# Kernel tuning notes

Measured on AMD Instinct MI355X. Metric: run time of the kernel, lower is better.

## Reference

```python
import jax, jax.numpy as jnp
import numpy as np
from jax import lax

D = 512        # datapathSize (= slow-net hidden size = embedding size)
H = 20         # nonlinearAfterSlowHiddenSize
V = 32000      # softmaxOutputHeadSize = xEmbeddingsNum
T = 1024       # sequence length (number of sequential fast-weight updates)


def setup_inputs() -> dict:
    key = jax.random.key(0)
    ks = jax.random.split(key, 12)
    inp = {}
    inp["tokens"] = jax.random.randint(ks[0], (T,), 0, V)
    inp["targets"] = jax.random.randint(ks[1], (T,), 0, V)
    # learned parameters
    inp["embed"] = jax.random.normal(ks[2], (V, D), dtype=jnp.float32)
    # fastWeightsInit = rand(D,D) * (1/D)
    inp["fw_init"] = jax.random.uniform(ks[3], (D, D), dtype=jnp.float32) * (1.0 / D)
    inp["eta"] = jnp.array(1.0, dtype=jnp.float32)
    inp["wa"] = jax.random.normal(ks[4], (D, D), dtype=jnp.float32) * 0.05
    inp["wb"] = jax.random.normal(ks[5], (D, D), dtype=jnp.float32) * 0.05
    # nonlinearAfterSlow: Linear(D,H) -> selu -> Linear(H,D); stored as (in,out)
    lim_a = 1.0 / np.sqrt(D)
    inp["mlp_aw"] = jax.random.uniform(ks[6], (D, H), dtype=jnp.float32, minval=-lim_a, maxval=lim_a)
    inp["mlp_ab"] = jax.random.uniform(ks[7], (H,), dtype=jnp.float32, minval=-lim_a, maxval=lim_a)
    lim_b = 1.0 / np.sqrt(H)
    inp["mlp_bw"] = jax.random.uniform(ks[8], (H, D), dtype=jnp.float32, minval=-lim_b, maxval=lim_b)
    inp["mlp_bb"] = jax.random.uniform(ks[9], (D,), dtype=jnp.float32, minval=-lim_b, maxval=lim_b)
    # logit head Linear(D, V)
    inp["head_w"] = jax.random.uniform(ks[10], (D, V), dtype=jnp.float32, minval=-lim_a, maxval=lim_a)
    inp["head_b"] = jax.random.uniform(ks[11], (V,), dtype=jnp.float32, minval=-lim_a, maxval=lim_a)
    return inp


def reference(tokens, targets, embed, fw_init, eta, wa, wb,
              mlp_aw, mlp_ab, mlp_bw, mlp_bb, head_w, head_b):
    xs = embed[tokens]  # [T, D]

    def step(fw, x):
        # SlowNetB.forwardAndUpdate for one token
        z0 = x @ wa                      # [D]
        z1 = x @ wb                      # [D]
        fw_new = jnp.tanh(fw + eta * jnp.outer(z0, z1))  # [D, D]
        y = x @ fw_new                   # [D]
        return fw_new, y

    _, ys = lax.scan(step, fw_init, xs)  # ys: [T, D]

    # NonlinearLayer (batched over T)
    h = jax.nn.selu(ys @ mlp_aw + mlp_ab) @ mlp_bw + mlp_bb  # [T, D]
    mixed = 0.5 * h + 0.5 * xs
    logits = mixed @ head_w + head_b     # [T, V]

    logp = jax.nn.log_softmax(logits, axis=-1)
    loss = -jnp.mean(jnp.take_along_axis(logp, targets[:, None], axis=1))
    return logits, loss
```

## Files before the change

kernel.cpp:

```cpp
#include <hip/hip_runtime.h>

#define D 512
#define H 20
#define V 32000
#define T 1024

typedef unsigned int uint;
typedef unsigned short ushort_t;
typedef __attribute__((ext_vector_type(8))) short short8;
typedef __attribute__((ext_vector_type(4))) float floatx4;

__device__ __forceinline__ unsigned short f2bf(float f) {
    unsigned u = __builtin_bit_cast(unsigned, f);
    u += 0x7fffu + ((u >> 16) & 1u);
    return (unsigned short)(u >> 16);
}

__device__ __forceinline__ float tanh_fast(float x) {
    float t = __builtin_amdgcn_exp2f(x * 2.8853900817779268f);
    float r = __builtin_amdgcn_rcpf(t + 1.0f);
    return __builtin_fmaf(-2.0f, r, 1.0f);
}

__global__ __launch_bounds__(256) void gather_kernel(const int* __restrict__ tokens,
                                                     const float* __restrict__ embed,
                                                     float* __restrict__ xs) {
    int idx = blockIdx.x * 256 + threadIdx.x;
    int row = idx >> 7;
    int c   = idx & 127;
    float4 v = ((const float4*)(embed + (long)tokens[row] * D))[c];
    ((float4*)xs)[idx] = v;
}

__global__ __launch_bounds__(256) void zgemm_kernel(const float* __restrict__ xs,
                                                    const float* __restrict__ wa,
                                                    const float* __restrict__ wb,
                                                    float* __restrict__ z0,
                                                    float* __restrict__ z1) {
    __shared__ float Xs[16 * 68];
    __shared__ float Ws[16 * 68];
    const int tid = threadIdx.x;
    const int n0 = blockIdx.x * 64, m0 = blockIdx.y * 64;
    const float* Wm = blockIdx.z ? wb : wa;
    float* Z = blockIdx.z ? z1 : z0;
    const int tx = tid & 15, ty = tid >> 4;
    const int xrow = tid >> 2, xkc = (tid & 3) * 4;
    const int wrow = tid >> 4, wc = (tid & 15) * 4;
    float acc[4][4] = {};
    for (int k0 = 0; k0 < D; k0 += 16) {
        float4 xv = *(const float4*)(xs + (long)(m0 + xrow) * D + k0 + xkc);
        float4 wv = *(const float4*)(Wm + (long)(k0 + wrow) * D + n0 + wc);
        Xs[(xkc + 0) * 68 + xrow] = xv.x;
        Xs[(xkc + 1) * 68 + xrow] = xv.y;
        Xs[(xkc + 2) * 68 + xrow] = xv.z;
        Xs[(xkc + 3) * 68 + xrow] = xv.w;
        *(float4*)(Ws + wrow * 68 + wc) = wv;
        __syncthreads();
#pragma unroll
        for (int k = 0; k < 16; k++) {
            float4 a = *(const float4*)(Xs + k * 68 + ty * 4);
            float4 b = *(const float4*)(Ws + k * 68 + tx * 4);
            float av[4] = {a.x, a.y, a.z, a.w};
            float bv[4] = {b.x, b.y, b.z, b.w};
#pragma unroll
            for (int r = 0; r < 4; r++)
#pragma unroll
                for (int c = 0; c < 4; c++)
                    acc[r][c] = __builtin_fmaf(av[r], bv[c], acc[r][c]);
        }
        __syncthreads();
    }
#pragma unroll
    for (int r = 0; r < 4; r++) {
        float4 v = {acc[r][0], acc[r][1], acc[r][2], acc[r][3]};
        *(float4*)(Z + (long)(m0 + ty * 4 + r) * D + n0 + tx * 4) = v;
    }
}

__global__ __launch_bounds__(512) void scan_kernel(const float* __restrict__ z0,
                                                   const float* __restrict__ z1,
                                                   const float* __restrict__ xs,
                                                   const float* __restrict__ fw_init,
                                                   const float* __restrict__ eta_p,
                                                   float* __restrict__ y) {
    const int tid = threadIdx.x;
    const int jj = tid & 1, ii = tid >> 1;
    const int j0 = blockIdx.x * 2;
    const int j = j0 + jj;
    const int wv = tid >> 6, lane = tid & 63;
    __shared__ float part[8 * 8 * 2];
    const float eta = *eta_p;
    float f0 = fw_init[(long)ii * D + j];
    float f1 = fw_init[(long)(ii + 256) * D + j];
    for (int t0 = 0; t0 < T; t0 += 8) {
        float za[8], zb[8], xa[8], xb[8], ez[8];
#pragma unroll
        for (int c = 0; c < 8; c++) {
            const long tr = (long)(t0 + c) * D;
            za[c] = z0[tr + ii];
            zb[c] = z0[tr + ii + 256];
            xa[c] = xs[tr + ii];
            xb[c] = xs[tr + ii + 256];
            ez[c] = z1[tr + j];
        }
        float p[8];
#pragma unroll
        for (int c = 0; c < 8; c++) {
            float e = eta * ez[c];
            f0 = tanh_fast(__builtin_fmaf(e, za[c], f0));
            f1 = tanh_fast(__builtin_fmaf(e, zb[c], f1));
            p[c] = xa[c] * f0 + xb[c] * f1;
        }
#pragma unroll
        for (int c = 0; c < 8; c++) {
            float v = p[c];
#pragma unroll
            for (int m = 2; m <= 32; m <<= 1) v += __shfl_xor(v, m, 64);
            p[c] = v;
        }
        if (lane < 2) {
#pragma unroll
            for (int c = 0; c < 8; c++) part[c * 16 + wv * 2 + lane] = p[c];
        }
        __syncthreads();
        if (tid < 16) {
            int c = tid >> 1, jx = tid & 1;
            float s = 0.f;
#pragma unroll
            for (int w = 0; w < 8; w++) s += part[c * 16 + w * 2 + jx];
            y[(long)(t0 + c) * D + j0 + jx] = s;
        }
        __syncthreads();
    }
}

__global__ __launch_bounds__(64) void mlp_mix_kernel(const float* __restrict__ y,
                                                     const float* __restrict__ xs,
                                                     const float* __restrict__ Aw,
                                                     const float* __restrict__ Ab,
                                                     const float* __restrict__ Bw,
                                                     const float* __restrict__ Bb,
                                                     unsigned short* __restrict__ mixed) {
    const int t = blockIdx.x, lane = threadIdx.x;
    __shared__ float Alds[H * D];
    __shared__ float h[H];
    for (int f = lane; f < H * D; f += 64) {
        float v = Aw[f];
        int d = f / H, j = f - d * H;
        Alds[j * D + d] = v;
    }
    float yr[8];
#pragma unroll
    for (int s = 0; s < 8; s++) yr[s] = y[(long)t * D + s * 64 + lane];
    __syncthreads();
    const float sc = 1.0507009873554805f, al = 1.6732632423543772f;
    for (int j = 0; j < H; j++) {
        float a = 0.f;
#pragma unroll
        for (int s = 0; s < 8; s++) a = __builtin_fmaf(yr[s], Alds[j * D + s * 64 + lane], a);
#pragma unroll
        for (int m = 1; m <= 32; m <<= 1) a += __shfl_xor(a, m, 64);
        if (lane == 0) {
            a += Ab[j];
            h[j] = a > 0.f ? sc * a : sc * al * (__expf(a) - 1.f);
        }
    }
    __syncthreads();
#pragma unroll
    for (int s = 0; s < 8; s++) {
        int d = s * 64 + lane;
        float o = Bb[d];
#pragma unroll
        for (int j = 0; j < H; j++) o = __builtin_fmaf(h[j], Bw[j * D + d], o);
        float mx = 0.5f * o + 0.5f * xs[(long)t * D + d];
        mixed[(long)t * D + d] = f2bf(mx);
    }
}

__global__ __launch_bounds__(256) void convert_wt_kernel(const float* __restrict__ head_w,
                                                         unsigned short* __restrict__ wt) {
    __shared__ float tile[64 * 68];
    const int n0 = blockIdx.x * 64, k0 = blockIdx.y * 64;
    const int tid = threadIdx.x;
#pragma unroll
    for (int s = 0; s < 4; s++) {
        int idx4 = s * 256 + tid;
        int r = idx4 >> 4, c4 = idx4 & 15;
        float4 v = *(const float4*)(head_w + (long)(k0 + r) * V + n0 + c4 * 4);
        *(float4*)(tile + r * 68 + c4 * 4) = v;
    }
    __syncthreads();
    const int rr = tid >> 2;
    const int cq = tid & 3;
    uint u[8];
#pragma unroll
    for (int p = 0; p < 8; p++) {
        float a = tile[(cq * 16 + p * 2 + 0) * 68 + rr];
        float b = tile[(cq * 16 + p * 2 + 1) * 68 + rr];
        u[p] = (uint)f2bf(a) | ((uint)f2bf(b) << 16);
    }
    unsigned short* ob = wt + (long)(n0 + rr) * D + k0 + cq * 16;
    uint4 v0 = {u[0], u[1], u[2], u[3]};
    uint4 v1 = {u[4], u[5], u[6], u[7]};
    *(uint4*)ob = v0;
    *((uint4*)ob + 1) = v1;
}

__global__ __launch_bounds__(256) void head_gemm_kernel(const unsigned short* __restrict__ A,
                                                        const unsigned short* __restrict__ Bt,
                                                        const float* __restrict__ bias,
                                                        float* __restrict__ C) {
    __shared__ unsigned short As[128 * 64];
    __shared__ unsigned short Bs[128 * 64];
    const int tid = threadIdx.x;
    const int mt = blockIdx.x & 7, nt = blockIdx.x >> 3;
    const int m0 = mt * 128, n0 = nt * 128;
    const int wave = tid >> 6, lane = tid & 63;
    const int wm = wave >> 1, wn = wave & 1;
    const int quad = lane >> 4, l15 = lane & 15;
    floatx4 acc[4][4] = {};
    for (int k0 = 0; k0 < D; k0 += 64) {
#pragma unroll
        for (int s = 0; s < 4; s++) {
            int idx = s * 256 + tid;
            int row = idx >> 3, slot = idx & 7;
            int gch = slot ^ (row & 7);
            const unsigned short* ga = A + (long)(m0 + row) * D + k0 + gch * 8;
            __builtin_amdgcn_global_load_lds(
                (const __attribute__((address_space(1))) unsigned int*)ga,
                (__attribute__((address_space(3))) unsigned int*)(As + idx * 8), 16, 0, 0);
            const unsigned short* gb = Bt + (long)(n0 + row) * D + k0 + gch * 8;
            __builtin_amdgcn_global_load_lds(
                (const __attribute__((address_space(1))) unsigned int*)gb,
                (__attribute__((address_space(3))) unsigned int*)(Bs + idx * 8), 16, 0, 0);
        }
        __syncthreads();
#pragma unroll
        for (int ks = 0; ks < 2; ks++) {
            short8 af[4], bfr[4];
            int q = ks * 4 + quad;
#pragma unroll
            for (int f = 0; f < 4; f++) {
                int ar = wm * 64 + f * 16 + l15;
                af[f] = *(const short8*)(As + ar * 64 + ((q ^ (ar & 7)) * 8));
                int br = wn * 64 + f * 16 + l15;
                bfr[f] = *(const short8*)(Bs + br * 64 + ((q ^ (br & 7)) * 8));
            }
#pragma unroll
            for (int fr = 0; fr < 4; fr++)
#pragma unroll
                for (int fc = 0; fc < 4; fc++)
                    acc[fr][fc] = __builtin_amdgcn_mfma_f32_16x16x32_bf16(af[fr], bfr[fc],
                                                                          acc[fr][fc], 0, 0, 0);
        }
        __syncthreads();
    }
#pragma unroll
    for (int fc = 0; fc < 4; fc++) {
        int n = n0 + wn * 64 + fc * 16 + l15;
        float b = bias[n];
#pragma unroll
        for (int fr = 0; fr < 4; fr++) {
            int mr = m0 + wm * 64 + fr * 16 + quad * 4;
#pragma unroll
            for (int r = 0; r < 4; r++)
                C[(long)(mr + r) * V + n] = acc[fr][fc][r] + b;
        }
    }
}

__device__ __forceinline__ void lse_upd(float& m, float& s, float v) {
    if (v > m) { s = s * __expf(m - v) + 1.f; m = v; }
    else       { s += __expf(v - m); }
}
__device__ __forceinline__ void lse_comb(float& m, float& s, float m2, float s2) {
    float M = fmaxf(m, m2);
    s = s * __expf(m - M) + s2 * __expf(m2 - M);
    m = M;
}

__global__ __launch_bounds__(256) void loss_rows_kernel(const float* __restrict__ logits,
                                                        const int* __restrict__ targets,
                                                        float* __restrict__ ws_loss) {
    const int t = blockIdx.x, tid = threadIdx.x;
    const float4* row = (const float4*)(logits + (long)t * V);
    float m = -INFINITY, s = 0.f;
    for (int i = tid; i < V / 4; i += 256) {
        float4 v = row[i];
        lse_upd(m, s, v.x); lse_upd(m, s, v.y); lse_upd(m, s, v.z); lse_upd(m, s, v.w);
    }
#pragma unroll
    for (int msk = 1; msk <= 32; msk <<= 1) {
        float m2 = __shfl_xor(m, msk, 64);
        float s2 = __shfl_xor(s, msk, 64);
        lse_comb(m, s, m2, s2);
    }
    __shared__ float sm[4], ss[4];
    if ((tid & 63) == 0) { sm[tid >> 6] = m; ss[tid >> 6] = s; }
    __syncthreads();
    if (tid == 0) {
        float M = sm[0], S = ss[0];
#pragma unroll
        for (int w = 1; w < 4; w++) lse_comb(M, S, sm[w], ss[w]);
        float lse = M + __logf(S);
        float lt = logits[(long)t * V + targets[t]];
        ws_loss[t] = lse - lt;
    }
}

__global__ __launch_bounds__(256) void loss_final_kernel(const float* __restrict__ ws_loss,
                                                         float* __restrict__ out) {
    const int tid = threadIdx.x;
    float s = 0.f;
    for (int i = tid; i < T; i += 256) s += ws_loss[i];
#pragma unroll
    for (int m = 1; m <= 32; m <<= 1) s += __shfl_xor(s, m, 64);
    __shared__ float red[4];
    if ((tid & 63) == 0) red[tid >> 6] = s;
    __syncthreads();
    if (tid == 0) out[0] = (red[0] + red[1] + red[2] + red[3]) * (1.f / (float)T);
}

extern "C" void kernel_launch(void* const* d_in, const int* in_sizes, int n_in,
                              void* d_out, int out_size, void* d_ws, size_t ws_size,
                              hipStream_t stream) {
    const int*   tokens  = (const int*)d_in[0];
    const int*   targets = (const int*)d_in[1];
    const float* embed   = (const float*)d_in[2];
    const float* fw_init = (const float*)d_in[3];
    const float* eta     = (const float*)d_in[4];
    const float* wa      = (const float*)d_in[5];
    const float* wb      = (const float*)d_in[6];
    const float* mlp_aw  = (const float*)d_in[7];
    const float* mlp_ab  = (const float*)d_in[8];
    const float* mlp_bw  = (const float*)d_in[9];
    const float* mlp_bb  = (const float*)d_in[10];
    const float* head_w  = (const float*)d_in[11];
    const float* head_b  = (const float*)d_in[12];
    float* out = (float*)d_out;

    char* ws = (char*)d_ws;
    float*          xs      = (float*)(ws + 0);
    float*          z0      = (float*)(ws + 2097152);
    float*          z1      = (float*)(ws + 4194304);
    float*          y       = (float*)(ws + 6291456);
    unsigned short* mixed   = (unsigned short*)(ws + 8388608);
    unsigned short* wt      = (unsigned short*)(ws + 9437184);
    float*          ws_loss = (float*)(ws + 42205184);

    convert_wt_kernel<<<dim3(V / 64, D / 64), 256, 0, stream>>>(head_w, wt);
    gather_kernel<<<(T * D / 4) / 256, 256, 0, stream>>>(tokens, embed, xs);
    zgemm_kernel<<<dim3(D / 64, T / 64, 2), 256, 0, stream>>>(xs, wa, wb, z0, z1);
    scan_kernel<<<D / 2, 512, 0, stream>>>(z0, z1, xs, fw_init, eta, y);
    mlp_mix_kernel<<<T, 64, 0, stream>>>(y, xs, mlp_aw, mlp_ab, mlp_bw, mlp_bb, mixed);
    head_gemm_kernel<<<(T / 128) * (V / 128), 256, 0, stream>>>(mixed, wt, head_b, out);
    loss_rows_kernel<<<T, 256, 0, stream>>>(out, targets, ws_loss);
    loss_final_kernel<<<1, 256, 0, stream>>>(ws_loss, out + (long)T * V);
}
```

Before: 646.1 us.

## Restructure scan to one column per block with prefetch and DPP reductions; split MLP

The scan kernel now assigns one output column per 256-thread block (512 blocks). It prefetches the next 8 timesteps of z/x into registers while the current chunk is reduced, and replaces shuffle-xor reductions with DPP row reductions. A double-buffered shared partial array removes one of the two barriers per chunk. The MLP is split into two elementwise-parallel kernels (hidden projection plus SELU, then output projection and mix) in place of one 64-thread block per token, adding an extra launch and a small intermediate buffer.

Result: faster. 567.0 us (-12.2%).

```diff
diff --git a/kernel.cpp b/kernel.cpp
--- a/kernel.cpp
+++ b/kernel.cpp
@@ -2,11 +2,11 @@
 
 #define D 512
 #define H 20
+#define HP 32
 #define V 32000
 #define T 1024
 
 typedef unsigned int uint;
-typedef unsigned short ushort_t;
 typedef __attribute__((ext_vector_type(8))) short short8;
 typedef __attribute__((ext_vector_type(4))) float floatx4;
 
@@ -20,6 +20,19 @@
     float t = __builtin_amdgcn_exp2f(x * 2.8853900817779268f);
     float r = __builtin_amdgcn_rcpf(t + 1.0f);
     return __builtin_fmaf(-2.0f, r, 1.0f);
+}
+
+template <int CTRL>
+__device__ __forceinline__ float dpp_add(float v) {
+    int x = __builtin_amdgcn_update_dpp(0, __builtin_bit_cast(int, v), CTRL, 0xf, 0xf, true);
+    return v + __builtin_bit_cast(float, x);
+}
+__device__ __forceinline__ float reduce16(float v) {
+    v = dpp_add<0xB1>(v);
+    v = dpp_add<0x4E>(v);
+    v = dpp_add<0x141>(v);
+    v = dpp_add<0x140>(v);
+    return v;
 }
 
 __global__ __launch_bounds__(256) void gather_kernel(const int* __restrict__ tokens,
@@ -77,32 +90,30 @@
     }
 }
 
-__global__ __launch_bounds__(512) void scan_kernel(const float* __restrict__ z0,
+__global__ __launch_bounds__(256) void scan_kernel(const float* __restrict__ z0,
                                                    const float* __restrict__ z1,
                                                    const float* __restrict__ xs,
                                                    const float* __restrict__ fw_init,
                                                    const float* __restrict__ eta_p,
                                                    float* __restrict__ y) {
     const int tid = threadIdx.x;
-    const int jj = tid & 1, ii = tid >> 1;
-    const int j0 = blockIdx.x * 2;
-    const int j = j0 + jj;
-    const int wv = tid >> 6, lane = tid & 63;
-    __shared__ float part[8 * 8 * 2];
+    const int j = blockIdx.x;
     const float eta = *eta_p;
-    float f0 = fw_init[(long)ii * D + j];
-    float f1 = fw_init[(long)(ii + 256) * D + j];
+    __shared__ float part2[2][8 * 16];
+    float f0 = fw_init[(long)tid * D + j];
+    float f1 = fw_init[(long)(tid + 256) * D + j];
+    float za[8], zb[8], xa[8], xb[8], ez[8];
+#pragma unroll
+    for (int c = 0; c < 8; c++) {
+        const long tr = (long)c * D;
+        za[c] = z0[tr + tid];
+        zb[c] = z0[tr + tid + 256];
+        xa[c] = xs[tr + tid];
+        xb[c] = xs[tr + tid + 256];
+        ez[c] = z1[tr + j];
+    }
+    int buf = 0;
     for (int t0 = 0; t0 < T; t0 += 8) {
-        float za[8], zb[8], xa[8], xb[8], ez[8];
-#pragma unroll
-        for (int c = 0; c < 8; c++) {
-            const long tr = (long)(t0 + c) * D;
-            za[c] = z0[tr + ii];
-            zb[c] = z0[tr + ii + 256];
-            xa[c] = xs[tr + ii];
-            xb[c] = xs[tr + ii + 256];
-            ez[c] = z1[tr + j];
-        }
         float p[8];
 #pragma unroll
         for (int c = 0; c < 8; c++) {
@@ -111,70 +122,63 @@
             f1 = tanh_fast(__builtin_fmaf(e, zb[c], f1));
             p[c] = xa[c] * f0 + xb[c] * f1;
         }
-#pragma unroll
-        for (int c = 0; c < 8; c++) {
-            float v = p[c];
-#pragma unroll
-            for (int m = 2; m <= 32; m <<= 1) v += __shfl_xor(v, m, 64);
-            p[c] = v;
-        }
-        if (lane < 2) {
-#pragma unroll
-            for (int c = 0; c < 8; c++) part[c * 16 + wv * 2 + lane] = p[c];
-        }
-        __syncthreads();
-        if (tid < 16) {
-            int c = tid >> 1, jx = tid & 1;
-            float s = 0.f;
-#pragma unroll
-            for (int w = 0; w < 8; w++) s += part[c * 16 + w * 2 + jx];
-            y[(long)(t0 + c) * D + j0 + jx] = s;
-        }
-        __syncthreads();
-    }
-}
-
-__global__ __launch_bounds__(64) void mlp_mix_kernel(const float* __restrict__ y,
-                                                     const float* __restrict__ xs,
-                                                     const float* __restrict__ Aw,
-                                                     const float* __restrict__ Ab,
-                                                     const float* __restrict__ Bw,
-                                                     const float* __restrict__ Bb,
-                                                     unsigned short* __restrict__ mixed) {
-    const int t = blockIdx.x, lane = threadIdx.x;
-    __shared__ float Alds[H * D];
-    __shared__ float h[H];
-    for (int f = lane; f < H * D; f += 64) {
-        float v = Aw[f];
-        int d = f / H, j = f - d * H;
-        Alds[j * D + d] = v;
-    }
-    float yr[8];
-#pragma unroll
-    for (int s = 0; s < 8; s++) yr[s] = y[(long)t * D + s * 64 + lane];
-    __syncthreads();
+        if (t0 + 8 < T) {
+#pragma unroll
+            for (int c = 0; c < 8; c++) {
+                const long tr = (long)(t0 + 8 + c) * D;
+                za[c] = z0[tr + tid];
+                zb[c] = z0[tr + tid + 256];
+                xa[c] = xs[tr + tid];
+                xb[c] = xs[tr + tid + 256];
+                ez[c] = z1[tr + j];
+            }
+        }
+#pragma unroll
+        for (int c = 0; c < 8; c++) p[c] = reduce16(p[c]);
+        if ((tid & 15) == 0) {
+            const int iiH = tid >> 4;
+#pragma unroll
+            for (int c = 0; c < 8; c++) part2[buf][c * 16 + iiH] = p[c];
+        }
+        __syncthreads();
+        if (tid < 128) {
+            const int c = tid >> 4, h = tid & 15;
+            float v = part2[buf][c * 16 + h];
+            v = reduce16(v);
+            if (h == 0) y[(long)(t0 + c) * D + j] = v;
+        }
+        buf ^= 1;
+    }
+}
+
+__global__ __launch_bounds__(256) void mlp_a_kernel(const float* __restrict__ y,
+                                                    const float* __restrict__ Aw,
+                                                    const float* __restrict__ Ab,
+                                                    float* __restrict__ hbuf) {
+    const int gid = blockIdx.x * 256 + threadIdx.x;
+    const int t = gid >> 5, jj = gid & 31;
+    if (jj >= H) return;
+    float a = 0.f;
+    const float* yr = y + (long)t * D;
+#pragma unroll 4
+    for (int d = 0; d < D; d++) a = __builtin_fmaf(yr[d], Aw[d * H + jj], a);
+    a += Ab[jj];
     const float sc = 1.0507009873554805f, al = 1.6732632423543772f;
-    for (int j = 0; j < H; j++) {
-        float a = 0.f;
-#pragma unroll
-        for (int s = 0; s < 8; s++) a = __builtin_fmaf(yr[s], Alds[j * D + s * 64 + lane], a);
-#pragma unroll
-        for (int m = 1; m <= 32; m <<= 1) a += __shfl_xor(a, m, 64);
-        if (lane == 0) {
-            a += Ab[j];
-            h[j] = a > 0.f ? sc * a : sc * al * (__expf(a) - 1.f);
-        }
-    }
-    __syncthreads();
-#pragma unroll
-    for (int s = 0; s < 8; s++) {
-        int d = s * 64 + lane;
-        float o = Bb[d];
-#pragma unroll
-        for (int j = 0; j < H; j++) o = __builtin_fmaf(h[j], Bw[j * D + d], o);
-        float mx = 0.5f * o + 0.5f * xs[(long)t * D + d];
-        mixed[(long)t * D + d] = f2bf(mx);
-    }
+    hbuf[t * HP + jj] = a > 0.f ? sc * a : sc * al * (__expf(a) - 1.f);
+}
+
+__global__ __launch_bounds__(256) void mlp_b_kernel(const float* __restrict__ hbuf,
+                                                    const float* __restrict__ xs,
+                                                    const float* __restrict__ Bw,
+                                                    const float* __restrict__ Bb,
+                                                    unsigned short* __restrict__ mixed) {
+    const int gid = blockIdx.x * 256 + threadIdx.x;
+    const int t = gid >> 9, d = gid & 511;
+    float o = Bb[d];
+    const float* hr = hbuf + (long)t * HP;
+#pragma unroll
+    for (int jj = 0; jj < H; jj++) o = __builtin_fmaf(hr[jj], Bw[jj * D + d], o);
+    mixed[gid] = f2bf(0.5f * o + 0.5f * xs[gid]);
 }
 
 __global__ __launch_bounds__(256) void convert_wt_kernel(const float* __restrict__ head_w,
@@ -347,12 +351,14 @@
     unsigned short* mixed   = (unsigned short*)(ws + 8388608);
     unsigned short* wt      = (unsigned short*)(ws + 9437184);
     float*          ws_loss = (float*)(ws + 42205184);
+    float*          hbuf    = (float*)(ws + 42209280);
 
     convert_wt_kernel<<<dim3(V / 64, D / 64), 256, 0, stream>>>(head_w, wt);
     gather_kernel<<<(T * D / 4) / 256, 256, 0, stream>>>(tokens, embed, xs);
     zgemm_kernel<<<dim3(D / 64, T / 64, 2), 256, 0, stream>>>(xs, wa, wb, z0, z1);
-    scan_kernel<<<D / 2, 512, 0, stream>>>(z0, z1, xs, fw_init, eta, y);
-    mlp_mix_kernel<<<T, 64, 0, stream>>>(y, xs, mlp_aw, mlp_ab, mlp_bw, mlp_bb, mixed);
+    scan_kernel<<<D, 256, 0, stream>>>(z0, z1, xs, fw_init, eta, y);
+    mlp_a_kernel<<<(T * HP) / 256, 256, 0, stream>>>(y, mlp_aw, mlp_ab, hbuf);
+    mlp_b_kernel<<<(T * D) / 256, 256, 0, stream>>>(hbuf, xs, mlp_bw, mlp_bb, mixed);
     head_gemm_kernel<<<(T / 128) * (V / 128), 256, 0, stream>>>(mixed, wt, head_b, out);
     loss_rows_kernel<<<T, 256, 0, stream>>>(out, targets, ws_loss);
     loss_final_kernel<<<1, 256, 0, stream>>>(ws_loss, out + (long)T * V);
```
